# Kernel tuning notes

Hardware: AMD Instinct MI355X
Metric: run time of the kernel (lower is better)

## Reference

```python
import jax, jax.numpy as jnp
import numpy as np

N, DIN, DOUT, R, E = 100000, 128, 256, 4, 600000
EPS = 1e-12


def setup_inputs() -> dict:
    key = jax.random.key(0)
    ks = jax.random.split(key, 8)
    x = jax.random.normal(ks[0], (N, DIN), dtype=jnp.float32)
    edge_index = jax.random.randint(ks[1], (R, 2, E), 0, N, dtype=jnp.int32)
    s1 = 1.0 / np.sqrt(DIN)
    s2 = 1.0 / np.sqrt(DOUT)
    W1n = jax.random.uniform(ks[2], (R, DOUT, DIN), jnp.float32, -s1, s1)
    W1r = jax.random.uniform(ks[3], (R, DOUT, DIN), jnp.float32, -s1, s1)
    b1 = jnp.zeros((R, DOUT), jnp.float32)
    W2n = jax.random.uniform(ks[4], (R, DOUT, DOUT), jnp.float32, -s2, s2)
    W2r = jax.random.uniform(ks[5], (R, DOUT, DOUT), jnp.float32, -s2, s2)
    b2 = jnp.zeros((R, DOUT), jnp.float32)
    return {"x": x, "edge_index": edge_index, "W1n": W1n, "b1": b1,
            "W1r": W1r, "W2n": W2n, "b2": b2, "W2r": W2r}


def _hetero_sage_layer(x, edge_index, Wn, b, Wr):
    # per-relation sum-aggregate of source features into destinations: [R, N, D]
    agg = jax.vmap(
        lambda e: jax.ops.segment_sum(x[e[0]], e[1], num_segments=N)
    )(edge_index)
    # SAGEConv: lin_l(agg) + bias + lin_r(x); mean across relations (to_hetero aggr='mean')
    out = (jnp.einsum('rnd,rod->rno', agg, Wn)
           + b[:, None, :]
           + jnp.einsum('nd,rod->rno', x, Wr))
    return out.mean(axis=0)  # [N, DOUT]


def _l2_normalize(h):
    nrm = jnp.sqrt(jnp.sum(h * h, axis=-1, keepdims=True))
    return h / jnp.maximum(nrm, EPS)


def reference(x, edge_index, W1n, b1, W1r, W2n, b2, W2r):
    h = _hetero_sage_layer(x, edge_index, W1n, b1, W1r)
    h = jax.nn.relu(_l2_normalize(h))  # dropout is identity in eval mode
    out = _hetero_sage_layer(h, edge_index, W2n, b2, W2r)
    return out  # x_dict['note']
```

## Files before the change

kernel.cpp:

```cpp
#include <hip/hip_runtime.h>
#include <hip/hip_bf16.h>

#define NN 100000
#define DIN 128
#define DOUT 256
#define RR 4
#define EE 600000
#define NB (RR * NN)
#define SCAN_BLKS 400
#define SCAN_CHUNK 1000

typedef __attribute__((ext_vector_type(4))) float f32x4;
typedef __attribute__((ext_vector_type(8))) short short8;
typedef __attribute__((ext_vector_type(2))) uint uint2v;

__device__ __forceinline__ float bf2f(ushort u) {
    union { unsigned int i; float f; } v; v.i = ((unsigned int)u) << 16; return v.f;
}
__device__ __forceinline__ ushort f2bf(float f) {
    union { float f; unsigned int i; } v; v.f = f;
    unsigned int r = v.i + 0x7fff + ((v.i >> 16) & 1);
    return (ushort)(r >> 16);
}

__device__ __forceinline__ void ld_g2l16(const void* g, void* l) {
    __builtin_amdgcn_global_load_lds(
        (const __attribute__((address_space(1))) void*)g,
        (__attribute__((address_space(3))) void*)l, 16, 0, 0);
}

__device__ __forceinline__ void store_w(ushort* W, int kd, int o, float s) {
    int cs = ((kd >> 3) & 7) ^ (o & 7);
    W[((size_t)(kd >> 6) * 256 + o) * 64 + cs * 8 + (kd & 7)] = f2bf(s);
}

#define W1ELEMS (5 * 128 * 256)
#define W2ELEMS (5 * 256 * 256)
__global__ void wprep_all(const float* __restrict__ W1n, const float* __restrict__ W1r,
                          const float* __restrict__ W2n, const float* __restrict__ W2r,
                          const float* __restrict__ b1, const float* __restrict__ b2,
                          ushort* __restrict__ W1c, ushort* __restrict__ W2c,
                          float* __restrict__ b1s, float* __restrict__ b2s) {
    int idx = blockIdx.x * blockDim.x + threadIdx.x;
    if (idx < W1ELEMS) {
        int p = idx / (128 * 256), rem = idx - p * (128 * 256);
        int k = rem >> 8, o = rem & 255;
        float s;
        if (p == 0) {
            s = 0.f;
            for (int r = 0; r < RR; ++r) s += W1r[(size_t)r * DOUT * DIN + (long)o * DIN + k];
        } else {
            s = W1n[(size_t)(p - 1) * DOUT * DIN + (long)o * DIN + k];
        }
        store_w(W1c, p * 128 + k, o, s * 0.25f);
        return;
    }
    idx -= W1ELEMS;
    if (idx < W2ELEMS) {
        int p = idx / (256 * 256), rem = idx - p * (256 * 256);
        int k = rem >> 8, o = rem & 255;
        float s;
        if (p == 0) {
            s = 0.f;
            for (int r = 0; r < RR; ++r) s += W2r[(size_t)r * DOUT * DOUT + (long)o * DOUT + k];
        } else {
            s = W2n[(size_t)(p - 1) * DOUT * DOUT + (long)o * DOUT + k];
        }
        store_w(W2c, p * 256 + k, o, s * 0.25f);
        return;
    }
    idx -= W2ELEMS;
    if (idx < 512) {
        int o = idx & 255;
        const float* b = (idx < 256) ? b1 : b2;
        float s = 0.f;
        for (int r = 0; r < RR; ++r) s += b[(long)r * 256 + o];
        ((idx < 256) ? b1s : b2s)[o] = s * 0.25f;
    }
}

__global__ void deg_count(const int* __restrict__ ei, int* __restrict__ deg) {
    int idx = blockIdx.x * blockDim.x + threadIdx.x;
    if (idx >= RR * (EE / 4)) return;
    int r = idx / (EE / 4), j = idx - r * (EE / 4);
    int4 d = ((const int4*)(ei + (size_t)r * 2 * EE + EE))[j];
    atomicAdd(&deg[r * NN + d.x], 1);
    atomicAdd(&deg[r * NN + d.y], 1);
    atomicAdd(&deg[r * NN + d.z], 1);
    atomicAdd(&deg[r * NN + d.w], 1);
}

__global__ __launch_bounds__(256) void scan_part(const int* __restrict__ deg,
                                                 int* __restrict__ bsum) {
    int b = blockIdx.x, t = threadIdx.x;
    int s = 0;
    for (int i = t; i < SCAN_CHUNK; i += 256) s += deg[b * SCAN_CHUNK + i];
    for (int o = 32; o > 0; o >>= 1) s += __shfl_down(s, o);
    __shared__ int red[4];
    if ((t & 63) == 0) red[t >> 6] = s;
    __syncthreads();
    if (t == 0) bsum[b] = red[0] + red[1] + red[2] + red[3];
}

__global__ __launch_bounds__(512) void scan_top(int* __restrict__ bsum) {
    __shared__ int v[512];
    int t = threadIdx.x;
    v[t] = (t < SCAN_BLKS) ? bsum[t] : 0;
    __syncthreads();
    for (int st = 1; st < 512; st <<= 1) {
        int tmp = (t >= st) ? v[t - st] : 0;
        __syncthreads();
        v[t] += tmp;
        __syncthreads();
    }
    if (t < SCAN_BLKS) bsum[t] = (t == 0) ? 0 : v[t - 1];
}

__global__ __launch_bounds__(256) void scan_final(int* __restrict__ degc,
                                                  const int* __restrict__ bsum,
                                                  int* __restrict__ off) {
    __shared__ int lv[1024];
    __shared__ int ts[256];
    int b = blockIdx.x, t = threadIdx.x;
    for (int i = t; i < 1024; i += 256)
        lv[i] = (i < SCAN_CHUNK) ? degc[b * SCAN_CHUNK + i] : 0;
    __syncthreads();
    int i0 = t * 4;
    int v0 = lv[i0], v1 = lv[i0 + 1], v2 = lv[i0 + 2], v3 = lv[i0 + 3];
    ts[t] = v0 + v1 + v2 + v3;
    __syncthreads();
    for (int st = 1; st < 256; st <<= 1) {
        int tmp = (t >= st) ? ts[t - st] : 0;
        __syncthreads();
        ts[t] += tmp;
        __syncthreads();
    }
    int run = bsum[b] + (t ? ts[t - 1] : 0);
    if (i0 < SCAN_CHUNK) {
        int base = b * SCAN_CHUNK + i0;
        off[base + 0] = run; degc[base + 0] = run; run += v0;
        off[base + 1] = run; degc[base + 1] = run; run += v1;
        off[base + 2] = run; degc[base + 2] = run; run += v2;
        off[base + 3] = run; degc[base + 3] = run; run += v3;
    }
    if (b == SCAN_BLKS - 1 && t == 255) off[NB] = bsum[b] + ts[255];
}

__global__ void fill_csr(const int* __restrict__ ei, int* __restrict__ cursor,
                         int* __restrict__ elist) {
    int idx = blockIdx.x * blockDim.x + threadIdx.x;
    if (idx >= RR * (EE / 4)) return;
    int r = idx / (EE / 4), j = idx - r * (EE / 4);
    int4 s = ((const int4*)(ei + (size_t)r * 2 * EE))[j];
    int4 d = ((const int4*)(ei + (size_t)r * 2 * EE + EE))[j];
    elist[atomicAdd(&cursor[r * NN + d.x], 1)] = s.x;
    elist[atomicAdd(&cursor[r * NN + d.y], 1)] = s.y;
    elist[atomicAdd(&cursor[r * NN + d.z], 1)] = s.z;
    elist[atomicAdd(&cursor[r * NN + d.w], 1)] = s.w;
}

__global__ void cvt_x(const float* __restrict__ x, ushort* __restrict__ XB) {
    int t = blockIdx.x * blockDim.x + threadIdx.x;
    if (t >= NN * 32) return;
    int n = t >> 5, c4 = (t & 31) * 4;
    float4 v = *(const float4*)&x[(size_t)n * 128 + c4];
    ushort4 o = {f2bf(v.x), f2bf(v.y), f2bf(v.z), f2bf(v.w)};
    *(ushort4*)&XB[(size_t)n * 128 + c4] = o;
}

template <int D>
__global__ void gather_bf16(const ushort* __restrict__ feat,
                            const int* __restrict__ elist, const int* __restrict__ off,
                            ushort* __restrict__ agg, int sout, int chunk) {
    constexpr int V = D / 64;
    int wv = blockIdx.x * 4 + (threadIdx.x >> 6);
    int lane = threadIdx.x & 63;
    if (wv >= NN * chunk) return;
    int n = wv / chunk, rl = wv - n * chunk;
    int b = rl * NN + n;
    int beg = off[b], end = off[b + 1];
    float acc[V];
#pragma unroll
    for (int v = 0; v < V; ++v) acc[v] = 0.f;
    int e = beg;
    for (; e + 2 <= end; e += 2) {
        int s0 = elist[e], s1 = elist[e + 1];
        const ushort* p0 = feat + (size_t)s0 * D + lane * V;
        const ushort* p1 = feat + (size_t)s1 * D + lane * V;
        if constexpr (V == 2) {
            ushort2 a = *(const ushort2*)p0, c = *(const ushort2*)p1;
            acc[0] += bf2f(a.x) + bf2f(c.x);
            acc[1] += bf2f(a.y) + bf2f(c.y);
        } else {
            ushort4 a = *(const ushort4*)p0, c = *(const ushort4*)p1;
            acc[0] += bf2f(a.x) + bf2f(c.x);
            acc[1] += bf2f(a.y) + bf2f(c.y);
            acc[2] += bf2f(a.z) + bf2f(c.z);
            acc[3] += bf2f(a.w) + bf2f(c.w);
        }
    }
    if (e < end) {
        int s0 = elist[e];
        const ushort* p0 = feat + (size_t)s0 * D + lane * V;
        if constexpr (V == 2) {
            ushort2 a = *(const ushort2*)p0;
            acc[0] += bf2f(a.x); acc[1] += bf2f(a.y);
        } else {
            ushort4 a = *(const ushort4*)p0;
            acc[0] += bf2f(a.x); acc[1] += bf2f(a.y);
            acc[2] += bf2f(a.z); acc[3] += bf2f(a.w);
        }
    }
    ushort* op = agg + (size_t)n * sout + rl * D + lane * V;
    if constexpr (V == 2) {
        uint u = (uint)f2bf(acc[0]) | ((uint)f2bf(acc[1]) << 16);
        __builtin_nontemporal_store(u, (uint*)op);
    } else {
        uint2v u;
        u.x = (uint)f2bf(acc[0]) | ((uint)f2bf(acc[1]) << 16);
        u.y = (uint)f2bf(acc[2]) | ((uint)f2bf(acc[3]) << 16);
        __builtin_nontemporal_store(u, (uint2v*)op);
    }
}

template <int MODE>
__global__ __launch_bounds__(256, 2) void gemm_fused(
    const ushort* __restrict__ F, int ldf, int K1,
    const ushort* __restrict__ G, int ldg, int K2,
    const ushort* __restrict__ W, const float* __restrict__ bias,
    void* __restrict__ Cout, int M) {
    __shared__ ushort lA[128 * 64];
    __shared__ ushort lB[256 * 64];
    __shared__ float rowsq[4][128];
    const int tid = threadIdx.x;
    const int w = tid >> 6, lane = tid & 63;
    const int row0 = blockIdx.x * 128;

    f32x4 acc[8][4];
#pragma unroll
    for (int i = 0; i < 8; ++i)
#pragma unroll
        for (int j = 0; j < 4; ++j) acc[i][j] = {0.f, 0.f, 0.f, 0.f};

    const int arow = lane >> 3;
    const int asrc = ((lane & 7) ^ arow) << 3;
    const int ldst = lane * 8;
    const ushort* aF[4]; const ushort* aG[4];
#pragma unroll
    for (int c = 0; c < 4; ++c) {
        int rg = row0 + w * 32 + c * 8 + arow;
        if (rg > M - 1) rg = M - 1;
        aF[c] = F + (size_t)rg * ldf + asrc;
        aG[c] = G + (size_t)rg * ldg + asrc;
    }
    const int nt = (K1 + K2) >> 6;

    for (int t = 0; t < nt; ++t) {
        __syncthreads();
        int kb = t << 6;
#pragma unroll
        for (int c = 0; c < 4; ++c) {
            const ushort* src = (kb < K1) ? (aF[c] + kb) : (aG[c] + (kb - K1));
            ld_g2l16(src, &lA[(w * 32 + c * 8) * 64 + ldst]);
        }
        const ushort* wb = W + (size_t)t * (256 * 64);
#pragma unroll
        for (int c = 0; c < 8; ++c)
            ld_g2l16(wb + (w * 64 + c * 8) * 64 + ldst, &lB[(w * 64 + c * 8) * 64 + ldst]);
        asm volatile("s_waitcnt vmcnt(0)" ::: "memory");
        __syncthreads();
        __builtin_amdgcn_s_setprio(1);
#pragma unroll
        for (int ks = 0; ks < 2; ++ks) {
            const int co = (((ks * 4 + (lane >> 4)) ^ (lane & 7)) << 3);
            short8 af[8];
#pragma unroll
            for (int rf = 0; rf < 8; ++rf)
                af[rf] = *(const short8*)&lA[(rf * 16 + (lane & 15)) * 64 + co];
#pragma unroll
            for (int cf = 0; cf < 4; ++cf) {
                short8 bf8 = *(const short8*)&lB[(w * 64 + cf * 16 + (lane & 15)) * 64 + co];
#pragma unroll
                for (int rf = 0; rf < 8; ++rf)
                    acc[rf][cf] = __builtin_amdgcn_mfma_f32_16x16x32_bf16(
                        af[rf], bf8, acc[rf][cf], 0, 0, 0);
            }
        }
        __builtin_amdgcn_s_setprio(0);
    }

#pragma unroll
    for (int cf = 0; cf < 4; ++cf) {
        float badd = bias[w * 64 + cf * 16 + (lane & 15)];
#pragma unroll
        for (int rf = 0; rf < 8; ++rf)
#pragma unroll
            for (int m = 0; m < 4; ++m) acc[rf][cf][m] += badd;
    }

    if constexpr (MODE == 0) {
        float* Cf = (float*)Cout;
#pragma unroll
        for (int cf = 0; cf < 4; ++cf) {
            int col = w * 64 + cf * 16 + (lane & 15);
#pragma unroll
            for (int rf = 0; rf < 8; ++rf)
#pragma unroll
                for (int m = 0; m < 4; ++m) {
                    int r = row0 + rf * 16 + (lane >> 4) * 4 + m;
                    if (r < M)
                        __builtin_nontemporal_store(acc[rf][cf][m],
                                                    &Cf[(size_t)r * 256 + col]);
                }
        }
    } else {
        float ss[8][4];
#pragma unroll
        for (int rf = 0; rf < 8; ++rf)
#pragma unroll
            for (int m = 0; m < 4; ++m) {
                float s = 0.f;
#pragma unroll
                for (int cf = 0; cf < 4; ++cf) s += acc[rf][cf][m] * acc[rf][cf][m];
#pragma unroll
                for (int o = 1; o < 16; o <<= 1) s += __shfl_xor(s, o);
                ss[rf][m] = s;
            }
        if ((lane & 15) == 0) {
#pragma unroll
            for (int rf = 0; rf < 8; ++rf)
#pragma unroll
                for (int m = 0; m < 4; ++m)
                    rowsq[w][rf * 16 + (lane >> 4) * 4 + m] = ss[rf][m];
        }
        __syncthreads();
        uint* HBw = (uint*)Cout;
#pragma unroll
        for (int rf = 0; rf < 8; ++rf)
#pragma unroll
            for (int m = 0; m < 4; ++m) {
                int tr = rf * 16 + (lane >> 4) * 4 + m;
                float tot = rowsq[0][tr] + rowsq[1][tr] + rowsq[2][tr] + rowsq[3][tr];
                float inv = 1.0f / fmaxf(sqrtf(tot), 1e-12f);
                int r = row0 + tr;
#pragma unroll
                for (int cf = 0; cf < 4; ++cf) {
                    float v = fmaxf(acc[rf][cf][m] * inv, 0.f);
                    uint u = f2bf(v);
                    uint pu = __shfl_xor(u, 1);
                    if (!(lane & 1) && r < M)
                        HBw[(size_t)r * 128 + ((w * 64 + cf * 16 + (lane & 15)) >> 1)] =
                            u | (pu << 16);
                }
            }
    }
}

extern "C" void kernel_launch(void* const* d_in, const int* in_sizes, int n_in,
                              void* d_out, int out_size, void* d_ws, size_t ws_size,
                              hipStream_t stream) {
    const float* x   = (const float*)d_in[0];
    const int*   ei  = (const int*)d_in[1];
    const float* W1n = (const float*)d_in[2];
    const float* b1  = (const float*)d_in[3];
    const float* W1r = (const float*)d_in[4];
    const float* W2n = (const float*)d_in[5];
    const float* b2  = (const float*)d_in[6];
    const float* W2r = (const float*)d_in[7];

    ushort* HB  = (ushort*)d_ws;
    ushort* G1  = HB + (size_t)NN * 256;
    ushort* G2  = G1 + (size_t)NN * 512;
    ushort* XB  = G2;
    int* elist  = (int*)(G2 + (size_t)NN * 1024);
    int* degc   = elist + (size_t)RR * EE;
    int* off    = degc + NB;
    int* bsum   = off + NB + 1;
    ushort* W1c = (ushort*)(bsum + 512);
    ushort* W2c = W1c + 640 * 256;
    float* b1s  = (float*)(W2c + 1280 * 256);
    float* b2s  = b1s + 256;

    hipMemsetAsync(degc, 0, (size_t)NB * sizeof(int), stream);
    deg_count<<<(RR * (EE / 4) + 255) / 256, 256, 0, stream>>>(ei, degc);
    scan_part<<<SCAN_BLKS, 256, 0, stream>>>(degc, bsum);
    scan_top<<<1, 512, 0, stream>>>(bsum);
    scan_final<<<SCAN_BLKS, 256, 0, stream>>>(degc, bsum, off);
    fill_csr<<<(RR * (EE / 4) + 255) / 256, 256, 0, stream>>>(ei, degc, elist);

    {
        int total = W1ELEMS + W2ELEMS + 512;
        wprep_all<<<(total + 255) / 256, 256, 0, stream>>>(W1n, W1r, W2n, W2r, b1, b2,
                                                           W1c, W2c, b1s, b2s);
    }
    cvt_x<<<(NN * 32 + 255) / 256, 256, 0, stream>>>(x, XB);

    const int ggrid = (NN + 127) / 128;

    gather_bf16<128><<<NN, 256, 0, stream>>>(XB, elist, off, G1, 512, RR);
    gemm_fused<1><<<ggrid, 256, 0, stream>>>(XB, 128, 128, G1, 512, 512, W1c, b1s, HB, NN);

    gather_bf16<256><<<NN, 256, 0, stream>>>(HB, elist, off, G2, 1024, RR);
    gemm_fused<0><<<ggrid, 256, 0, stream>>>(HB, 256, 256, G2, 1024, 1024, W2c, b2s,
                                             d_out, NN);
}
```

Baseline: 867.1 us.

## Triple-buffer GEMM LDS tiles with async prefetch and unroll gather by four

The fused GEMM now keeps three LDS stages, prefetching tile t+2 while computing tile t, and waits with a partial vmcnt instead of draining all loads each iteration. This is meant to hide global-to-LDS latency behind the MFMA work. LDS use rises to about 147KB, so launch bounds drop to one block per CU, which lowers occupancy. Separately, the gather kernel unrolls its edge loop to four independent row loads per iteration to raise memory-level parallelism.

```diff
diff --git a/kernel.cpp b/kernel.cpp
--- a/kernel.cpp
+++ b/kernel.cpp
@@ -182,31 +182,35 @@
     float acc[V];
 #pragma unroll
     for (int v = 0; v < V; ++v) acc[v] = 0.f;
+    const ushort* fbase = feat + lane * V;
     int e = beg;
-    for (; e + 2 <= end; e += 2) {
-        int s0 = elist[e], s1 = elist[e + 1];
-        const ushort* p0 = feat + (size_t)s0 * D + lane * V;
-        const ushort* p1 = feat + (size_t)s1 * D + lane * V;
+    for (; e + 4 <= end; e += 4) {
+        int s0 = elist[e], s1 = elist[e + 1], s2 = elist[e + 2], s3 = elist[e + 3];
         if constexpr (V == 2) {
-            ushort2 a = *(const ushort2*)p0, c = *(const ushort2*)p1;
-            acc[0] += bf2f(a.x) + bf2f(c.x);
-            acc[1] += bf2f(a.y) + bf2f(c.y);
+            ushort2 a0 = *(const ushort2*)(fbase + (size_t)s0 * D);
+            ushort2 a1 = *(const ushort2*)(fbase + (size_t)s1 * D);
+            ushort2 a2 = *(const ushort2*)(fbase + (size_t)s2 * D);
+            ushort2 a3 = *(const ushort2*)(fbase + (size_t)s3 * D);
+            acc[0] += (bf2f(a0.x) + bf2f(a1.x)) + (bf2f(a2.x) + bf2f(a3.x));
+            acc[1] += (bf2f(a0.y) + bf2f(a1.y)) + (bf2f(a2.y) + bf2f(a3.y));
         } else {
-            ushort4 a = *(const ushort4*)p0, c = *(const ushort4*)p1;
-            acc[0] += bf2f(a.x) + bf2f(c.x);
-            acc[1] += bf2f(a.y) + bf2f(c.y);
-            acc[2] += bf2f(a.z) + bf2f(c.z);
-            acc[3] += bf2f(a.w) + bf2f(c.w);
-        }
-    }
-    if (e < end) {
+            ushort4 a0 = *(const ushort4*)(fbase + (size_t)s0 * D);
+            ushort4 a1 = *(const ushort4*)(fbase + (size_t)s1 * D);
+            ushort4 a2 = *(const ushort4*)(fbase + (size_t)s2 * D);
+            ushort4 a3 = *(const ushort4*)(fbase + (size_t)s3 * D);
+            acc[0] += (bf2f(a0.x) + bf2f(a1.x)) + (bf2f(a2.x) + bf2f(a3.x));
+            acc[1] += (bf2f(a0.y) + bf2f(a1.y)) + (bf2f(a2.y) + bf2f(a3.y));
+            acc[2] += (bf2f(a0.z) + bf2f(a1.z)) + (bf2f(a2.z) + bf2f(a3.z));
+            acc[3] += (bf2f(a0.w) + bf2f(a1.w)) + (bf2f(a2.w) + bf2f(a3.w));
+        }
+    }
+    for (; e < end; ++e) {
         int s0 = elist[e];
-        const ushort* p0 = feat + (size_t)s0 * D + lane * V;
         if constexpr (V == 2) {
-            ushort2 a = *(const ushort2*)p0;
+            ushort2 a = *(const ushort2*)(fbase + (size_t)s0 * D);
             acc[0] += bf2f(a.x); acc[1] += bf2f(a.y);
         } else {
-            ushort4 a = *(const ushort4*)p0;
+            ushort4 a = *(const ushort4*)(fbase + (size_t)s0 * D);
             acc[0] += bf2f(a.x); acc[1] += bf2f(a.y);
             acc[2] += bf2f(a.z); acc[3] += bf2f(a.w);
         }
@@ -223,14 +227,14 @@
     }
 }
 
+#define TILE_USH ((128 + 256) * 64)
 template <int MODE>
-__global__ __launch_bounds__(256, 2) void gemm_fused(
+__global__ __launch_bounds__(256, 1) void gemm_fused(
     const ushort* __restrict__ F, int ldf, int K1,
     const ushort* __restrict__ G, int ldg, int K2,
     const ushort* __restrict__ W, const float* __restrict__ bias,
     void* __restrict__ Cout, int M) {
-    __shared__ ushort lA[128 * 64];
-    __shared__ ushort lB[256 * 64];
+    __shared__ ushort lds[3][TILE_USH];
     __shared__ float rowsq[4][128];
     const int tid = threadIdx.x;
     const int w = tid >> 6, lane = tid & 63;
@@ -255,20 +259,37 @@
     }
     const int nt = (K1 + K2) >> 6;
 
-    for (int t = 0; t < nt; ++t) {
-        __syncthreads();
+    auto STAGE = [&](int b, int t) {
         int kb = t << 6;
+        ushort* dA = &lds[b][0];
+        ushort* dB = &lds[b][128 * 64];
 #pragma unroll
         for (int c = 0; c < 4; ++c) {
             const ushort* src = (kb < K1) ? (aF[c] + kb) : (aG[c] + (kb - K1));
-            ld_g2l16(src, &lA[(w * 32 + c * 8) * 64 + ldst]);
+            ld_g2l16(src, dA + (w * 32 + c * 8) * 64 + ldst);
         }
         const ushort* wb = W + (size_t)t * (256 * 64);
 #pragma unroll
         for (int c = 0; c < 8; ++c)
-            ld_g2l16(wb + (w * 64 + c * 8) * 64 + ldst, &lB[(w * 64 + c * 8) * 64 + ldst]);
-        asm volatile("s_waitcnt vmcnt(0)" ::: "memory");
-        __syncthreads();
+            ld_g2l16(wb + (w * 64 + c * 8) * 64 + ldst, dB + (w * 64 + c * 8) * 64 + ldst);
+    };
+
+    STAGE(0, 0);
+    if (nt > 1) STAGE(1, 1);
+
+    int cur = 0;
+    for (int t = 0; t < nt; ++t) {
+        if (t + 1 < nt) {
+            asm volatile("s_waitcnt vmcnt(12)" ::: "memory");
+        } else {
+            asm volatile("s_waitcnt vmcnt(0)" ::: "memory");
+        }
+        __builtin_amdgcn_s_barrier();
+        __builtin_amdgcn_sched_barrier(0);
+        if (t + 2 < nt) {
+            int nb = cur + 2; if (nb >= 3) nb -= 3;
+            STAGE(nb, t + 2);
+        }
         __builtin_amdgcn_s_setprio(1);
 #pragma unroll
         for (int ks = 0; ks < 2; ++ks) {
@@ -276,10 +297,11 @@
             short8 af[8];
 #pragma unroll
             for (int rf = 0; rf < 8; ++rf)
-                af[rf] = *(const short8*)&lA[(rf * 16 + (lane & 15)) * 64 + co];
+                af[rf] = *(const short8*)&lds[cur][(rf * 16 + (lane & 15)) * 64 + co];
 #pragma unroll
             for (int cf = 0; cf < 4; ++cf) {
-                short8 bf8 = *(const short8*)&lB[(w * 64 + cf * 16 + (lane & 15)) * 64 + co];
+                short8 bf8 = *(const short8*)&lds[cur]
+                                 [128 * 64 + (w * 64 + cf * 16 + (lane & 15)) * 64 + co];
 #pragma unroll
                 for (int rf = 0; rf < 8; ++rf)
                     acc[rf][cf] = __builtin_amdgcn_mfma_f32_16x16x32_bf16(
@@ -287,6 +309,7 @@
             }
         }
         __builtin_amdgcn_s_setprio(0);
+        ++cur; if (cur == 3) cur = 0;
     }
 
 #pragma unroll
```

Measured after the change: 929.1 us. +7.1%, slower.
